# Performance work log

Measured on AMD Instinct MI355X. Metric: run time of the kernel, lower is better.

Reference implementation:

```python
import jax, jax.numpy as jnp
import numpy as np

EPS = 1e-08


def _center(K):
    # H K H with H = I - 11^T/n, expressed as O(n^2) double mean-subtraction
    rm = K.mean(axis=-1, keepdims=True)
    cm = K.mean(axis=-2, keepdims=True)
    tm = K.mean(axis=(-1, -2), keepdims=True)
    return K - rm - cm + tm


def setup_inputs() -> dict:
    key = jax.random.key(0)
    k1, k2 = jax.random.split(key)
    L, B, n, d = 5, 8, 1024, 64
    teacher = jax.random.normal(k1, (L, B, n, d), dtype=jnp.float32)
    student = jax.random.normal(k2, (L, B, n, d), dtype=jnp.float32)
    return {"teacher": teacher, "student": student}


def reference(teacher, student):
    # teacher, student: [L, B, n, d]  (internal=True, dim>=3 branch)
    cX = _center(jnp.einsum('lbnd,lbmd->lbnm', teacher, teacher))  # [L,B,n,n]
    cY = _center(jnp.einsum('lbnd,lbmd->lbnm', student, student))  # [L,B,n,n]
    hsic_xy = jnp.sum(cX * cY, axis=(-1, -2))  # [L,B]
    var_x = jnp.sqrt(jnp.sum(cX * cX, axis=(-1, -2)))  # [L,B]
    var_y = jnp.sqrt(jnp.sum(cY * cY, axis=(-1, -2)))  # [L,B]
    ratio = jnp.abs(hsic_xy / (var_x * var_y))  # [L,B]
    loss_per_layer = -jnp.log(ratio.mean(axis=-1) + EPS)  # [L]
    return loss_per_layer.mean()  # sum over layers / length
```

## Files before the change

kernel.cpp:

```cpp
#include <hip/hip_runtime.h>
#include <math.h>

#define LL 5
#define BB 8
#define NN 1024
#define DD 64
#define LB 40
#define SPLIT 16
#define KC (NN / SPLIT)
#define ZC (2 * DD)
#define NQ 3

#define GP_SZ (LB * SPLIT * NQ * 4096)
#define SP_SZ (LB * SPLIT * ZC)
#define ACC_OFF (GP_SZ + SP_SZ)

typedef short short8 __attribute__((ext_vector_type(8)));
typedef float floatx4 __attribute__((ext_vector_type(4)));

__device__ __forceinline__ unsigned short f2bf(float f) {
    union { float f; unsigned u; } v; v.f = f;
    const unsigned u = v.u;
    return (unsigned short)((u + 0x7FFFu + ((u >> 16) & 1u)) >> 16);
}
__device__ __forceinline__ float bf2f(unsigned short h) {
    union { unsigned u; float f; } v; v.u = ((unsigned)h) << 16; return v.f;
}

__device__ __forceinline__ short8 read_frag(const short* Zt, int tbase, int lane, int k0) {
    const int c = tbase + (lane & 15);
    const int o = (k0 >> 3) + (lane >> 4);
    const int oct = (o ^ ((c + (c >> 4)) & 15)) & 7;
    return *(const short8*)(Zt + c * 64 + (oct << 3));
}

__global__ __launch_bounds__(256) void gram_kernel(const float* __restrict__ X,
                                                   const float* __restrict__ Y,
                                                   float* __restrict__ Gp,
                                                   float* __restrict__ Sp) {
    __shared__ short Zt[ZC * KC];
    __shared__ float cscr[8][ZC];

    const int lb = blockIdx.y, nc = blockIdx.x, tid = threadIdx.x;
    const int r0 = nc * KC;
    const float4* X4 = (const float4*)(X + (size_t)lb * NN * DD);
    const float4* Y4 = (const float4*)(Y + (size_t)lb * NN * DD);

    const int col4 = tid & 31;
    const int rb = tid >> 5;
    float4 v[8];
#pragma unroll
    for (int m = 0; m < 8; ++m) {
        const int row = 8 * rb + m;
        v[m] = (col4 < 16) ? X4[(size_t)(r0 + row) * 16 + col4]
                           : Y4[(size_t)(r0 + row) * 16 + (col4 - 16)];
    }

#pragma unroll
    for (int e = 0; e < 4; ++e) {
        const int c = 4 * col4 + e;
        short8 w8;
        float cs = 0.f;
#pragma unroll
        for (int m = 0; m < 8; ++m) {
            const float fv = (e == 0) ? v[m].x : (e == 1) ? v[m].y : (e == 2) ? v[m].z : v[m].w;
            const unsigned short b = f2bf(fv);
            cs += bf2f(b);
            w8[m] = (short)b;
        }
        const int oct = (rb ^ ((c + (c >> 4)) & 15)) & 7;
        *(short8*)(Zt + c * 64 + (oct << 3)) = w8;
        cscr[rb][c] = cs;
    }
    __syncthreads();
    if (tid < ZC) {
        float s = 0.f;
#pragma unroll
        for (int g = 0; g < 8; ++g) s += cscr[g][tid];
        Sp[(lb * SPLIT + nc) * ZC + tid] = s;
    }

    const int lane = tid & 63, w = tid >> 6;

    floatx4 acc[2][8];
#pragma unroll
    for (int i = 0; i < 2; ++i)
#pragma unroll
        for (int j = 0; j < 8; ++j) acc[i][j] = (floatx4){0.f, 0.f, 0.f, 0.f};

#pragma unroll
    for (int k0 = 0; k0 < KC; k0 += 32) {
        short8 af[2], bfr[8];
#pragma unroll
        for (int i = 0; i < 2; ++i) af[i] = read_frag(Zt, (2 * w + i) * 16, lane, k0);
#pragma unroll
        for (int j = 0; j < 8; ++j) bfr[j] = read_frag(Zt, j * 16, lane, k0);
#pragma unroll
        for (int i = 0; i < 2; ++i)
#pragma unroll
            for (int j = 0; j < 8; ++j)
                acc[i][j] = __builtin_amdgcn_mfma_f32_16x16x32_bf16(af[i], bfr[j], acc[i][j], 0, 0, 0);
    }

    float* Gb = Gp + (size_t)(lb * SPLIT + nc) * (NQ * 4096);
    const int g = lane >> 4, cl = lane & 15;
    if (w < 2) {
#pragma unroll
        for (int i = 0; i < 2; ++i)
#pragma unroll
            for (int j = 0; j < 8; ++j) {
                const int slab = (j < 4) ? 0 : 1;
                const int qcol = (j & 3) * 16 + cl;
#pragma unroll
                for (int r = 0; r < 4; ++r) {
                    const int qrow = (2 * w + i) * 16 + g * 4 + r;
                    Gb[slab * 4096 + qrow * 64 + qcol] = acc[i][j][r];
                }
            }
    } else {
#pragma unroll
        for (int i = 0; i < 2; ++i)
#pragma unroll
            for (int j = 4; j < 8; ++j) {
                const int qcol = (j - 4) * 16 + cl;
#pragma unroll
                for (int r = 0; r < 4; ++r) {
                    const int qrow = (2 * (w - 2) + i) * 16 + g * 4 + r;
                    Gb[2 * 4096 + qrow * 64 + qcol] = acc[i][j][r];
                }
            }
    }
}

__global__ __launch_bounds__(256) void reduce_kernel(const float* __restrict__ Gp,
                                                     const float* __restrict__ Sp,
                                                     float* __restrict__ Acc2) {
    const int b = blockIdx.x;
    const int lb = b / (NQ * 4);
    const int rem = b % (NQ * 4);
    const int q = rem >> 2, seg = rem & 3;
    const int tid = threadIdx.x;

    __shared__ float stot[ZC];
    __shared__ float red[4];

    if (tid < ZC) {
        float s = 0.f;
#pragma unroll
        for (int sp = 0; sp < SPLIT; ++sp) s += Sp[(lb * SPLIT + sp) * ZC + tid];
        stot[tid] = s;
    }
    __syncthreads();

    const int idx0 = seg * 256 + tid;
    float4 g = make_float4(0.f, 0.f, 0.f, 0.f);
#pragma unroll
    for (int sp = 0; sp < SPLIT; ++sp) {
        const float4 p = *(const float4*)&Gp[((size_t)(lb * SPLIT + sp) * NQ + q) * 4096 + idx0 * 4];
        g.x += p.x; g.y += p.y; g.z += p.z; g.w += p.w;
    }
    const int row = idx0 >> 4, col0 = (idx0 & 15) * 4;
    const int rowbase = (q == 2) ? 64 : 0;
    const int colbase = (q == 0) ? 0 : 64;
    const float inv_n = 1.0f / (float)NN;
    const float srow = stot[rowbase + row] * inv_n;
    const float ga[4] = {g.x, g.y, g.z, g.w};
    float sq = 0.f;
#pragma unroll
    for (int e = 0; e < 4; ++e) {
        const float cv = ga[e] - srow * stot[colbase + col0 + e];
        sq += cv * cv;
    }
#pragma unroll
    for (int off = 32; off; off >>= 1) sq += __shfl_down(sq, off);
    const int wave = tid >> 6;
    if ((tid & 63) == 0) red[wave] = sq;
    __syncthreads();
    if (tid == 0)
        Acc2[lb * 12 + q * 4 + seg] = red[0] + red[1] + red[2] + red[3];
}

__global__ void final_kernel(const float* __restrict__ Acc2, float* __restrict__ out) {
    const int tid = threadIdx.x;
    float v = 0.0f;
    if (tid < LB) {
        float vxx = 0.f, hxy = 0.f, vyy = 0.f;
#pragma unroll
        for (int s = 0; s < 4; ++s) {
            vxx += Acc2[tid * 12 + s];
            hxy += Acc2[tid * 12 + 4 + s];
            vyy += Acc2[tid * 12 + 8 + s];
        }
        v = fabsf(hxy / (sqrtf(vxx) * sqrtf(vyy)));
    }
    v += __shfl_xor(v, 1);
    v += __shfl_xor(v, 2);
    v += __shfl_xor(v, 4);
    float loss = 0.0f;
#pragma unroll
    for (int l = 0; l < LL; ++l) {
        const float sl = __shfl(v, l * BB);
        loss += -logf(sl * (1.0f / (float)BB) + 1e-8f);
    }
    if (tid == 0) out[0] = loss * (1.0f / (float)LL);
}

extern "C" void kernel_launch(void* const* d_in, const int* in_sizes, int n_in,
                              void* d_out, int out_size, void* d_ws, size_t ws_size,
                              hipStream_t stream) {
    const float* teacher = (const float*)d_in[0];
    const float* student = (const float*)d_in[1];
    float* ws = (float*)d_ws;
    float* Gp = ws;
    float* Sp = ws + GP_SZ;
    float* Acc2 = ws + ACC_OFF;

    dim3 grid1(SPLIT, LB);
    gram_kernel<<<grid1, 256, 0, stream>>>(teacher, student, Gp, Sp);
    reduce_kernel<<<LB * NQ * 4, 256, 0, stream>>>(Gp, Sp, Acc2);
    final_kernel<<<1, 64, 0, stream>>>(Acc2, (float*)d_out);
}
```

Baseline: 78.08 us.

## Store partial d×d Gram slabs as packed bf16 and skip unused MFMA tiles

The per-split partial Gram products written to workspace are converted to bf16 and packed two rows per 32-bit word, which halves the global write and read traffic between the gram and reduce kernels. The reduce kernel unpacks the pairs and accumulates in fp32. Waves 2-3 no longer load B fragments or issue MFMAs for the j<4 tiles they never stored. The cost is extra rounding error in the partial sums, which could hurt accuracy of the centered norms and the HSIC ratio.

New measurement: 77.30 us. About the same (-1.0%).

```diff
diff --git a/kernel.cpp b/kernel.cpp
--- a/kernel.cpp
+++ b/kernel.cpp
@@ -11,9 +11,10 @@
 #define ZC (2 * DD)
 #define NQ 3
 
-#define GP_SZ (LB * SPLIT * NQ * 4096)
-#define SP_SZ (LB * SPLIT * ZC)
-#define ACC_OFF (GP_SZ + SP_SZ)
+#define GP_SHORTS (LB * SPLIT * NQ * 4096)
+#define GP_FLOATS (GP_SHORTS / 2)
+#define SP_OFF GP_FLOATS
+#define ACC_OFF (GP_FLOATS + LB * SPLIT * ZC)
 
 typedef short short8 __attribute__((ext_vector_type(8)));
 typedef float floatx4 __attribute__((ext_vector_type(4)));
@@ -25,6 +26,12 @@
 }
 __device__ __forceinline__ float bf2f(unsigned short h) {
     union { unsigned u; float f; } v; v.u = ((unsigned)h) << 16; return v.f;
+}
+__device__ __forceinline__ float bflo(unsigned u) {
+    union { unsigned u; float f; } v; v.u = u << 16; return v.f;
+}
+__device__ __forceinline__ float bfhi(unsigned u) {
+    union { unsigned u; float f; } v; v.u = u & 0xFFFF0000u; return v.f;
 }
 
 __device__ __forceinline__ short8 read_frag(const short* Zt, int tbase, int lane, int k0) {
@@ -36,7 +43,7 @@
 
 __global__ __launch_bounds__(256) void gram_kernel(const float* __restrict__ X,
                                                    const float* __restrict__ Y,
-                                                   float* __restrict__ Gp,
+                                                   unsigned* __restrict__ Gp,
                                                    float* __restrict__ Sp) {
     __shared__ short Zt[ZC * KC];
     __shared__ float cscr[8][ZC];
@@ -81,6 +88,7 @@
     }
 
     const int lane = tid & 63, w = tid >> 6;
+    const int jbeg = (w < 2) ? 0 : 4;
 
     floatx4 acc[2][8];
 #pragma unroll
@@ -94,45 +102,36 @@
 #pragma unroll
         for (int i = 0; i < 2; ++i) af[i] = read_frag(Zt, (2 * w + i) * 16, lane, k0);
 #pragma unroll
-        for (int j = 0; j < 8; ++j) bfr[j] = read_frag(Zt, j * 16, lane, k0);
+        for (int j = 0; j < 8; ++j)
+            if (j >= jbeg) bfr[j] = read_frag(Zt, j * 16, lane, k0);
 #pragma unroll
         for (int i = 0; i < 2; ++i)
 #pragma unroll
             for (int j = 0; j < 8; ++j)
-                acc[i][j] = __builtin_amdgcn_mfma_f32_16x16x32_bf16(af[i], bfr[j], acc[i][j], 0, 0, 0);
-    }
-
-    float* Gb = Gp + (size_t)(lb * SPLIT + nc) * (NQ * 4096);
+                if (j >= jbeg)
+                    acc[i][j] = __builtin_amdgcn_mfma_f32_16x16x32_bf16(af[i], bfr[j], acc[i][j], 0, 0, 0);
+    }
+
+    unsigned* Gb = Gp + (size_t)(lb * SPLIT + nc) * (NQ * 2048);
     const int g = lane >> 4, cl = lane & 15;
-    if (w < 2) {
-#pragma unroll
-        for (int i = 0; i < 2; ++i)
-#pragma unroll
-            for (int j = 0; j < 8; ++j) {
-                const int slab = (j < 4) ? 0 : 1;
-                const int qcol = (j & 3) * 16 + cl;
-#pragma unroll
-                for (int r = 0; r < 4; ++r) {
-                    const int qrow = (2 * w + i) * 16 + g * 4 + r;
-                    Gb[slab * 4096 + qrow * 64 + qcol] = acc[i][j][r];
-                }
+#pragma unroll
+    for (int i = 0; i < 2; ++i)
+#pragma unroll
+        for (int j = 0; j < 8; ++j) {
+            if (j < jbeg) continue;
+            const int slab = (w < 2) ? ((j < 4) ? 0 : 1) : 2;
+            const int qrow0 = (w < 2 ? (2 * w + i) : (2 * (w - 2) + i)) * 16 + g * 4;
+            const int qcol = (j & 3) * 16 + cl;
+            if (w < 2 || j >= 4) {
+                const unsigned lo = (unsigned)f2bf(acc[i][j][0]) | ((unsigned)f2bf(acc[i][j][1]) << 16);
+                const unsigned hi = (unsigned)f2bf(acc[i][j][2]) | ((unsigned)f2bf(acc[i][j][3]) << 16);
+                Gb[slab * 2048 + (qrow0 >> 1) * 64 + qcol] = lo;
+                Gb[slab * 2048 + ((qrow0 >> 1) + 1) * 64 + qcol] = hi;
             }
-    } else {
-#pragma unroll
-        for (int i = 0; i < 2; ++i)
-#pragma unroll
-            for (int j = 4; j < 8; ++j) {
-                const int qcol = (j - 4) * 16 + cl;
-#pragma unroll
-                for (int r = 0; r < 4; ++r) {
-                    const int qrow = (2 * (w - 2) + i) * 16 + g * 4 + r;
-                    Gb[2 * 4096 + qrow * 64 + qcol] = acc[i][j][r];
-                }
-            }
-    }
-}
-
-__global__ __launch_bounds__(256) void reduce_kernel(const float* __restrict__ Gp,
+        }
+}
+
+__global__ __launch_bounds__(256) void reduce_kernel(const unsigned* __restrict__ Gp,
                                                      const float* __restrict__ Sp,
                                                      float* __restrict__ Acc2) {
     const int b = blockIdx.x;
@@ -152,25 +151,30 @@
     }
     __syncthreads();
 
-    const int idx0 = seg * 256 + tid;
-    float4 g = make_float4(0.f, 0.f, 0.f, 0.f);
+    const int u0 = seg * 512 + tid * 2;
+    const int rp = u0 >> 6;
+    const int c0 = u0 & 63;
+
+    float g00 = 0.f, g10 = 0.f, g01 = 0.f, g11 = 0.f;
 #pragma unroll
     for (int sp = 0; sp < SPLIT; ++sp) {
-        const float4 p = *(const float4*)&Gp[((size_t)(lb * SPLIT + sp) * NQ + q) * 4096 + idx0 * 4];
-        g.x += p.x; g.y += p.y; g.z += p.z; g.w += p.w;
-    }
-    const int row = idx0 >> 4, col0 = (idx0 & 15) * 4;
+        const uint2 p = *(const uint2*)&Gp[((size_t)(lb * SPLIT + sp) * NQ + q) * 2048 + u0];
+        g00 += bflo(p.x); g10 += bfhi(p.x);
+        g01 += bflo(p.y); g11 += bfhi(p.y);
+    }
     const int rowbase = (q == 2) ? 64 : 0;
     const int colbase = (q == 0) ? 0 : 64;
     const float inv_n = 1.0f / (float)NN;
-    const float srow = stot[rowbase + row] * inv_n;
-    const float ga[4] = {g.x, g.y, g.z, g.w};
+    const float sr0 = stot[rowbase + 2 * rp] * inv_n;
+    const float sr1 = stot[rowbase + 2 * rp + 1] * inv_n;
+    const float sc0 = stot[colbase + c0];
+    const float sc1 = stot[colbase + c0 + 1];
     float sq = 0.f;
-#pragma unroll
-    for (int e = 0; e < 4; ++e) {
-        const float cv = ga[e] - srow * stot[colbase + col0 + e];
-        sq += cv * cv;
-    }
+    { const float cv = g00 - sr0 * sc0; sq += cv * cv; }
+    { const float cv = g10 - sr1 * sc0; sq += cv * cv; }
+    { const float cv = g01 - sr0 * sc1; sq += cv * cv; }
+    { const float cv = g11 - sr1 * sc1; sq += cv * cv; }
+
 #pragma unroll
     for (int off = 32; off; off >>= 1) sq += __shfl_down(sq, off);
     const int wave = tid >> 6;
@@ -211,8 +215,8 @@
     const float* teacher = (const float*)d_in[0];
     const float* student = (const float*)d_in[1];
     float* ws = (float*)d_ws;
-    float* Gp = ws;
-    float* Sp = ws + GP_SZ;
+    unsigned* Gp = (unsigned*)ws;
+    float* Sp = ws + SP_OFF;
     float* Acc2 = ws + ACC_OFF;
 
     dim3 grid1(SPLIT, LB);
```
